# Optimization experiments

Hardware: AMD Instinct MI355X
Metric: run time of the kernel (lower is better)

Reference implementation:

```python
import jax, jax.numpy as jnp
import numpy as np

B, C, H, W = 4, 2048, 32, 32


def conv1x1(x, Wt, b):
    # 1x1 conv == per-pixel matmul over channels
    return jnp.einsum('oc,bchw->bohw', Wt, x) + b[None, :, None, None]


def cross_attention(Q, K, V):
    b, c, h, w = Q.shape
    q = Q.reshape(b, c, h * w)   # [B, C, N]
    k = K.reshape(b, c, h * w)
    v = V.reshape(b, c, h * w)
    scores = jnp.einsum('bcn,bcm->bnm', q, k) / jnp.sqrt(jnp.asarray(c, jnp.float32))
    attn = jax.nn.softmax(scores, axis=-1)          # [B, N, N]
    out = jnp.einsum('bcm,bnm->bcn', v, attn)       # V @ attn^T
    return out.reshape(b, c, h, w)


def setup_inputs() -> dict:
    key = jax.random.key(0)
    ks = jax.random.split(key, 14)
    d = {
        'F_rgb': jax.random.normal(ks[0], (B, C, H, W), jnp.float32),
        'F_indices': jax.random.normal(ks[1], (B, C, H, W), jnp.float32),
    }
    names = ['q_rgb', 'k_rgb', 'v_rgb', 'q_ind', 'k_ind', 'v_ind']
    for i, n in enumerate(names):
        d['W_' + n] = jax.random.normal(ks[2 + 2 * i], (C, C), jnp.float32) * 0.02
        d['b_' + n] = jax.random.normal(ks[3 + 2 * i], (C,), jnp.float32) * 0.01
    return d


def reference(F_rgb, F_indices, W_q_rgb, b_q_rgb, W_k_rgb, b_k_rgb, W_v_rgb, b_v_rgb,
              W_q_ind, b_q_ind, W_k_ind, b_k_ind, W_v_ind, b_v_ind):
    # RGB queries attend over index features
    Q_rgb = conv1x1(F_rgb, W_q_rgb, b_q_rgb)
    K_ind = conv1x1(F_indices, W_k_ind, b_k_ind)
    V_ind = conv1x1(F_indices, W_v_ind, b_v_ind)
    F_rgb_attended = cross_attention(Q_rgb, K_ind, V_ind)
    # Index queries attend over RGB features
    Q_ind = conv1x1(F_indices, W_q_ind, b_q_ind)
    K_rgb = conv1x1(F_rgb, W_k_rgb, b_k_rgb)
    V_rgb = conv1x1(F_rgb, W_v_rgb, b_v_rgb)
    F_ind_attended = cross_attention(Q_ind, K_rgb, V_rgb)
    F_final = F_rgb_attended + F_ind_attended
    attention_weights = jnp.stack([F_rgb_attended, F_ind_attended], axis=1)  # [B,2,C,H,W]
    # pre_attention_outputs is an identity passthrough of the inputs
    return (F_final, F_rgb, F_indices, attention_weights)
```

## Files before the change

### kernel.cpp

```cpp
#include <hip/hip_runtime.h>

typedef __bf16 bf16x8 __attribute__((ext_vector_type(8)));
typedef float  f32x4  __attribute__((ext_vector_type(4)));
typedef unsigned short u16;

__device__ __forceinline__ u16 f2bf(float f) {
  unsigned u = __builtin_bit_cast(unsigned, f);
  u += 0x7fffu + ((u >> 16) & 1u);
  return (u16)(u >> 16);
}
__device__ __forceinline__ float bf2f(u16 h) {
  return __builtin_bit_cast(float, (unsigned)h << 16);
}

using gvoid = __attribute__((address_space(1))) void;
using svoid = __attribute__((address_space(3))) void;
__device__ __forceinline__ void load_lds16(const void* g, void* s) {
  __builtin_amdgcn_global_load_lds((const gvoid*)g, (svoid*)s, 16, 0, 0);
}

__global__ void transpose_cvt(const float* __restrict__ Fr, const float* __restrict__ Fi,
                              u16* __restrict__ FTr, u16* __restrict__ FTi,
                              float* __restrict__ Or, float* __restrict__ Oi) {
  __shared__ float tile[32][33];
  const int b = blockIdx.z & 3;
  const bool ind = (blockIdx.z >= 4);
  const float* F = ind ? Fi : Fr;
  u16* FT = ind ? FTi : FTr;
  float* O = ind ? Oi : Or;
  const int n0 = blockIdx.x * 32, c0 = blockIdx.y * 32;
  const long boff = (long)b * 2048 * 1024;
  const float* Fb = F + boff;
  float* Ob = O + boff;
  u16* FTb = FT + (long)b * 1024 * 2048;
  const int tx = threadIdx.x, ty = threadIdx.y;
#pragma unroll
  for (int i = 0; i < 4; ++i) {
    const long idx = (long)(c0 + ty + i * 8) * 1024 + n0 + tx;
    float v = Fb[idx];
    tile[ty + i * 8][tx] = v;
    Ob[idx] = v;
  }
  __syncthreads();
#pragma unroll
  for (int i = 0; i < 4; ++i)
    FTb[(long)(n0 + ty + i * 8) * 2048 + c0 + tx] = f2bf(tile[tx][ty + i * 8]);
}

__global__ void cvt6(const float* __restrict__ s0, const float* __restrict__ s1,
                     const float* __restrict__ s2, const float* __restrict__ s3,
                     const float* __restrict__ s4, const float* __restrict__ s5,
                     u16* __restrict__ dst) {
  const int blk = blockIdx.x;
  const int chunk = blk >> 12;
  const int i = (blk & 4095) * 256 + threadIdx.x;
  const float* src;
  switch (chunk) {
    case 0: src = s0; break; case 1: src = s1; break; case 2: src = s2; break;
    case 3: src = s3; break; case 4: src = s4; break; default: src = s5; break;
  }
  float4 v = ((const float4*)src)[i];
  ushort4 o;
  o.x = f2bf(v.x); o.y = f2bf(v.y); o.z = f2bf(v.z); o.w = f2bf(v.w);
  ((ushort4*)(dst + (long)chunk * 4194304))[i] = o;
}


#define BAR_ do { asm volatile("" ::: "memory"); __builtin_amdgcn_s_barrier(); \
                  asm volatile("" ::: "memory"); } while (0)
#define SB0 __builtin_amdgcn_sched_barrier(0)
#define LGK0 asm volatile("s_waitcnt lgkmcnt(0)" ::: "memory")
#define VMW6 asm volatile("s_waitcnt vmcnt(6)" ::: "memory")

#define b0A0 0
#define b0A1 16384
#define b0B0 32768
#define b0B1 49152
#define b1A0 65536
#define b1A1 81920
#define b1B0 98304
#define b1B1 114688

#define STG(Mp, ld, row0, kt, off)                                                 \
  do {                                                                             \
    load_lds16(Mp + (long)((row0) + w * 8 + srow) * (ld) + (kt) * 64 + scol,       \
               sm + (off) + w * 1024);                                             \
    load_lds16(Mp + (long)((row0) + 64 + w * 8 + srow) * (ld) + (kt) * 64 + scol,  \
               sm + (off) + 8192 + w * 1024);                                      \
  } while (0)

#define RDA(off)                                                                   \
  _Pragma("unroll") for (int fm = 0; fm < 4; ++fm)                                 \
  _Pragma("unroll") for (int ks = 0; ks < 2; ++ks)                                 \
    fa[fm][ks] = *(const bf16x8*)(sm + (off) + aoff[fm] + kin[ks]);

#define RDB(off, dst)                                                              \
  _Pragma("unroll") for (int fn = 0; fn < 2; ++fn)                                 \
  _Pragma("unroll") for (int ks = 0; ks < 2; ++ks)                                 \
    dst[fn][ks] = *(const bf16x8*)(sm + (off) + boff[fn] + kin[ks]);

#define MMQ2(qa)                                                                   \
  __builtin_amdgcn_s_setprio(1);                                                   \
  _Pragma("unroll") for (int ks = 0; ks < 2; ++ks)                                 \
  _Pragma("unroll") for (int fm = 0; fm < 4; ++fm) {                               \
    _Pragma("unroll") for (int fn = 0; fn < 2; ++fn)                               \
      acc[qa][0][fm][fn] = __builtin_amdgcn_mfma_f32_16x16x32_bf16(                \
          fa[fm][ks], fb0[fn][ks], acc[qa][0][fm][fn], 0, 0, 0);                   \
    _Pragma("unroll") for (int fn = 0; fn < 2; ++fn)                               \
      acc[qa][1][fm][fn] = __builtin_amdgcn_mfma_f32_16x16x32_bf16(                \
          fa[fm][ks], fb1[fn][ks], acc[qa][1][fm][fn], 0, 0, 0);                   \
  }                                                                                \
  __builtin_amdgcn_s_setprio(0);

template <int OUT_BF16, int BIAS_MODE, int KSPLIT>
__global__ __launch_bounds__(512, 2) void gemm256(
    const u16* __restrict__ A0p, const u16* __restrict__ B0p, void* __restrict__ D0p,
    const float* __restrict__ ba0, const float* __restrict__ bb0,
    const u16* __restrict__ A1p, const u16* __restrict__ B1p, void* __restrict__ D1p,
    const float* __restrict__ ba1, const float* __restrict__ bb1,
    long sKH, int zsplit, int K, int lda, int ldb, int ldd,
    long sA, long sB, long sD) {
  __shared__ __attribute__((aligned(128))) char sm[131072];
  const int gx = gridDim.x, gy = gridDim.y;
  const int nwg = gx * gy * (int)gridDim.z;
  const int lin = blockIdx.x + gx * (blockIdx.y + gy * blockIdx.z);
  const int qch = nwg >> 3;
  int swzid = (lin & 7) * qch + (lin >> 3);
  const int bx = swzid % gx; swzid /= gx;
  const int by = swzid % gy;
  int zb = swzid / gy;
  int kh = 0;
  if (KSPLIT) { kh = zb >> 3; zb &= 7; }
  const bool s1 = (zb >= zsplit);
  const int zz = s1 ? zb - zsplit : zb;
  const u16* Ag = (s1 ? A1p : A0p) + (long)zz * sA + (long)kh * K;
  const u16* Bg = (s1 ? B1p : B0p) + (long)zz * sB + (long)kh * K;
  char* Dg = (char*)(s1 ? D1p : D0p) + (long)zz * sD * (OUT_BF16 ? 2 : 4)
           + (KSPLIT ? (long)kh * sKH : 0L);
  const float* ba = s1 ? ba1 : ba0;
  const float* bb = s1 ? bb1 : bb0;
  const int m0 = by * 256, n0 = bx * 256;
  const int t = threadIdx.x, w = t >> 6, l = t & 63;
  const int wr = w >> 2, wc = w & 3;
  const int lm = l & 15, lk = l >> 4;
  const int swz = (l & 7) << 4;
  const int srow = l >> 3;
  const int scol = ((l & 7) ^ srow) << 3;
  int aoff[4], boff[2], kin[2];
#pragma unroll
  for (int fm = 0; fm < 4; ++fm) aoff[fm] = (wr * 64 + fm * 16 + lm) * 128;
#pragma unroll
  for (int fn = 0; fn < 2; ++fn) boff[fn] = (wc * 32 + fn * 16 + lm) * 128;
  kin[0] = (lk * 16) ^ swz;
  kin[1] = (64 + lk * 16) ^ swz;

  f32x4 acc[2][2][4][2] = {};
  bf16x8 fa[4][2], fb0[2][2], fb1[2][2];

  const int nt = K >> 6;

  STG(Ag, lda, m0,       0, b0A0);
  STG(Bg, ldb, n0,       0, b0B0);
  STG(Bg, ldb, n0 + 128, 0, b0B1);
  STG(Ag, lda, m0 + 128, 0, b0A1);
  STG(Ag, lda, m0,       1, b1A0);
  STG(Bg, ldb, n0,       1, b1B0);
  STG(Bg, ldb, n0 + 128, 1, b1B1);
  VMW6;
  BAR_;

  for (int v = 0; v < nt; v += 2) {
    const int t2 = (v + 2 < nt) ? v + 2 : nt - 1;
    const int t3 = (v + 3 < nt) ? v + 3 : nt - 1;
    STG(Ag, lda, m0 + 128, v + 1, b1A1);
    RDA(b0A0); RDB(b0B0, fb0); RDB(b0B1, fb1);
    BAR_; LGK0; SB0; MMQ2(0);
    STG(Ag, lda, m0, t2, b0A0);
    STG(Bg, ldb, n0, t2, b0B0);
    STG(Bg, ldb, n0 + 128, t2, b0B1);
    RDA(b0A1);
    VMW6;
    BAR_; LGK0; SB0; MMQ2(1);
    STG(Ag, lda, m0 + 128, t2, b0A1);
    RDA(b1A0); RDB(b1B0, fb0); RDB(b1B1, fb1);
    BAR_; LGK0; SB0; MMQ2(0);
    STG(Ag, lda, m0, t3, b1A0);
    STG(Bg, ldb, n0, t3, b1B0);
    STG(Bg, ldb, n0 + 128, t3, b1B1);
    RDA(b1A1);
    VMW6;
    BAR_; LGK0; SB0; MMQ2(1);
  }

#pragma unroll
  for (int qa = 0; qa < 2; ++qa)
#pragma unroll
    for (int qb = 0; qb < 2; ++qb)
#pragma unroll
      for (int fm = 0; fm < 4; ++fm)
#pragma unroll
        for (int fn = 0; fn < 2; ++fn) {
          const int row0 = m0 + qa * 128 + wr * 64 + fm * 16 + lk * 4;
          const int col  = n0 + qb * 128 + wc * 32 + fn * 16 + lm;
          float cb = 0.f;
          if (BIAS_MODE == 1) cb = (col < 2048) ? ba[col] : bb[col - 2048];
          f32x4 vv = acc[qa][qb][fm][fn];
#pragma unroll
          for (int j = 0; j < 4; ++j) {
            float x = vv[j] + cb;
            if (BIAS_MODE == 2) x += ba[row0 + j];
            const long idx = (long)(row0 + j) * ldd + col;
            if (OUT_BF16) ((u16*)Dg)[idx] = f2bf(x);
            else          ((float*)Dg)[idx] = x;
          }
        }
}

__global__ void softmax_rows2(const u16* __restrict__ S0, const u16* __restrict__ S1,
                              u16* __restrict__ P, float alpha) {
  const long row = blockIdx.x;
  const int t = threadIdx.x, l = t & 63, w = t >> 6;
  ushort4 a = ((const ushort4*)(S0 + row * 1024))[t];
  ushort4 b = ((const ushort4*)(S1 + row * 1024))[t];
  float v0 = bf2f(a.x) + bf2f(b.x);
  float v1 = bf2f(a.y) + bf2f(b.y);
  float v2 = bf2f(a.z) + bf2f(b.z);
  float v3 = bf2f(a.w) + bf2f(b.w);
  __shared__ float red[8];
  float m = fmaxf(fmaxf(v0, v1), fmaxf(v2, v3));
#pragma unroll
  for (int off = 32; off; off >>= 1) m = fmaxf(m, __shfl_xor(m, off));
  if (l == 0) red[w] = m;
  __syncthreads();
  m = fmaxf(fmaxf(red[0], red[1]), fmaxf(red[2], red[3]));
  float e0 = __expf((v0 - m) * alpha);
  float e1 = __expf((v1 - m) * alpha);
  float e2 = __expf((v2 - m) * alpha);
  float e3 = __expf((v3 - m) * alpha);
  float s = e0 + e1 + e2 + e3;
#pragma unroll
  for (int off = 32; off; off >>= 1) s += __shfl_xor(s, off);
  if (l == 0) red[4 + w] = s;
  __syncthreads();
  s = red[4] + red[5] + red[6] + red[7];
  const float inv = 1.0f / s;
  ushort4 o;
  o.x = f2bf(e0 * inv); o.y = f2bf(e1 * inv);
  o.z = f2bf(e2 * inv); o.w = f2bf(e3 * inv);
  ((ushort4*)(P + row * 1024))[t] = o;
}

__global__ void final_add(const float4* __restrict__ aw, float4* __restrict__ dst) {
  const long i = (long)blockIdx.x * 256 + threadIdx.x;
  const long b = i >> 19;
  const long r = i & 524287;
  float4 a = aw[b * 1048576 + r];
  float4 c = aw[b * 1048576 + 524288 + r];
  float4 o;
  o.x = a.x + c.x; o.y = a.y + c.y; o.z = a.z + c.z; o.w = a.w + c.w;
  dst[i] = o;
}

extern "C" void kernel_launch(void* const* d_in, const int* in_sizes, int n_in,
                              void* d_out, int out_size, void* d_ws, size_t ws_size,
                              hipStream_t stream) {
  (void)in_sizes; (void)n_in; (void)out_size; (void)ws_size;
  const float* F_rgb = (const float*)d_in[0];
  const float* F_ind = (const float*)d_in[1];
  const float* bq_rgb = (const float*)d_in[3];
  const float* bk_rgb = (const float*)d_in[5];
  const float* bv_rgb = (const float*)d_in[7];
  const float* bq_ind = (const float*)d_in[9];
  const float* bk_ind = (const float*)d_in[11];
  const float* bv_ind = (const float*)d_in[13];

  char* ws = (char*)d_ws;
  u16* FT_rgb  = (u16*)(ws);
  u16* FT_ind  = (u16*)(ws + 16777216);
  u16* S1c     = (u16*)(ws);
  u16* Wall    = (u16*)(ws + 33554432);
  u16* Wqk_rgb = Wall;
  u16* Wqk_ind = (u16*)(ws + 50331648);
  u16* Wv_rgb  = (u16*)(ws + 67108864);
  u16* Wv_ind  = (u16*)(ws + 75497472);
  u16* QKT_rgb = (u16*)(ws + 83886080);
  u16* QKT_ind = (u16*)(ws + 117440512);
  u16* V_rgb   = (u16*)(ws + 150994944);
  u16* V_ind   = (u16*)(ws + 167772160);
  u16* S0c     = (u16*)(ws + 184549376);
  u16* P       = (u16*)(ws + 218103808);

  float* out       = (float*)d_out;
  float* out_final = out;
  float* out_Frgb  = out + 8388608;
  float* out_Find  = out + 16777216;
  float* AW        = out + 25165824;

  transpose_cvt<<<dim3(32, 64, 8), dim3(32, 8), 0, stream>>>(
      F_rgb, F_ind, FT_rgb, FT_ind, out_Frgb, out_Find);
  cvt6<<<24576, 256, 0, stream>>>((const float*)d_in[2], (const float*)d_in[4],
                                  (const float*)d_in[8], (const float*)d_in[10],
                                  (const float*)d_in[6], (const float*)d_in[12], Wall);

  gemm256<1, 1, 0><<<dim3(16, 4, 8), 512, 0, stream>>>(
      FT_rgb, Wqk_rgb, QKT_rgb, bq_rgb, bk_rgb,
      FT_ind, Wqk_ind, QKT_ind, bq_ind, bk_ind,
      0L, 4, 2048, 2048, 2048, 4096, 2097152L, 0L, 4194304L);

  gemm256<1, 2, 0><<<dim3(4, 8, 8), 512, 0, stream>>>(
      Wv_rgb, FT_rgb, V_rgb, bv_rgb, bv_rgb,
      Wv_ind, FT_ind, V_ind, bv_ind, bv_ind,
      0L, 4, 2048, 2048, 2048, 1024, 0L, 2097152L, 2097152L);

  gemm256<1, 0, 1><<<dim3(4, 4, 16), 512, 0, stream>>>(
      QKT_rgb, QKT_ind + 2048, S0c, nullptr, nullptr,
      QKT_ind, QKT_rgb + 2048, S0c + 4194304, nullptr, nullptr,
      (long)((char*)S1c - (char*)S0c), 4, 1024, 4096, 4096, 1024,
      4194304L, 4194304L, 1048576L);

  softmax_rows2<<<8192, 256, 0, stream>>>(S0c, S1c, P, 0.02209708691207961f);

  gemm256<0, 0, 0><<<dim3(4, 8, 8), 512, 0, stream>>>(
      V_ind, P, AW, nullptr, nullptr,
      V_rgb, P + 4194304, AW + 2097152, nullptr, nullptr,
      0L, 4, 1024, 1024, 1024, 1024, 2097152L, 1048576L, 4194304L);

  final_add<<<8192, 256, 0, stream>>>((const float4*)AW, (float4*)out_final);
}
```

Baseline: 329.4 us.

## Merge prep kernels and use smaller 128-tile GEMM for attention matmuls

Fuses the input transpose/convert kernel and the weight conversion kernel into one launch using extra grid z-slices. Adds a simpler 128x128-tile, 256-thread GEMM without multi-buffering and uses it for the scores GEMM and the attention-times-V GEMM. This gives those smaller GEMMs more blocks to fill the GPU's compute units, but gives up the deeper pipelining of the 256-tile kernel because each k-step waits on its loads before computing.

New measurement: 364.4 us. 10.6% more time.

```diff
diff --git a/kernel.cpp b/kernel.cpp
--- a/kernel.cpp
+++ b/kernel.cpp
@@ -19,9 +19,29 @@
   __builtin_amdgcn_global_load_lds((const gvoid*)g, (svoid*)s, 16, 0, 0);
 }
 
-__global__ void transpose_cvt(const float* __restrict__ Fr, const float* __restrict__ Fi,
-                              u16* __restrict__ FTr, u16* __restrict__ FTi,
-                              float* __restrict__ Or, float* __restrict__ Oi) {
+__global__ void prep(const float* __restrict__ Fr, const float* __restrict__ Fi,
+                     u16* __restrict__ FTr, u16* __restrict__ FTi,
+                     float* __restrict__ Or, float* __restrict__ Oi,
+                     const float* __restrict__ s0, const float* __restrict__ s1,
+                     const float* __restrict__ s2, const float* __restrict__ s3,
+                     const float* __restrict__ s4, const float* __restrict__ s5,
+                     u16* __restrict__ Wall) {
+  const int tx = threadIdx.x, ty = threadIdx.y;
+  if (blockIdx.z >= 8) {
+    const int gi = (blockIdx.z - 8) * 2048 + blockIdx.y * 32 + blockIdx.x;
+    const int chunk = gi >> 12;
+    const int i = (gi & 4095) * 256 + ty * 32 + tx;
+    const float* src;
+    switch (chunk) {
+      case 0: src = s0; break; case 1: src = s1; break; case 2: src = s2; break;
+      case 3: src = s3; break; case 4: src = s4; break; default: src = s5; break;
+    }
+    float4 v = ((const float4*)src)[i];
+    ushort4 o;
+    o.x = f2bf(v.x); o.y = f2bf(v.y); o.z = f2bf(v.z); o.w = f2bf(v.w);
+    ((ushort4*)(Wall + (long)chunk * 4194304))[i] = o;
+    return;
+  }
   __shared__ float tile[32][33];
   const int b = blockIdx.z & 3;
   const bool ind = (blockIdx.z >= 4);
@@ -33,7 +53,6 @@
   const float* Fb = F + boff;
   float* Ob = O + boff;
   u16* FTb = FT + (long)b * 1024 * 2048;
-  const int tx = threadIdx.x, ty = threadIdx.y;
 #pragma unroll
   for (int i = 0; i < 4; ++i) {
     const long idx = (long)(c0 + ty + i * 8) * 1024 + n0 + tx;
@@ -45,24 +64,6 @@
 #pragma unroll
   for (int i = 0; i < 4; ++i)
     FTb[(long)(n0 + ty + i * 8) * 2048 + c0 + tx] = f2bf(tile[tx][ty + i * 8]);
-}
-
-__global__ void cvt6(const float* __restrict__ s0, const float* __restrict__ s1,
-                     const float* __restrict__ s2, const float* __restrict__ s3,
-                     const float* __restrict__ s4, const float* __restrict__ s5,
-                     u16* __restrict__ dst) {
-  const int blk = blockIdx.x;
-  const int chunk = blk >> 12;
-  const int i = (blk & 4095) * 256 + threadIdx.x;
-  const float* src;
-  switch (chunk) {
-    case 0: src = s0; break; case 1: src = s1; break; case 2: src = s2; break;
-    case 3: src = s3; break; case 4: src = s4; break; default: src = s5; break;
-  }
-  float4 v = ((const float4*)src)[i];
-  ushort4 o;
-  o.x = f2bf(v.x); o.y = f2bf(v.y); o.z = f2bf(v.z); o.w = f2bf(v.w);
-  ((ushort4*)(dst + (long)chunk * 4194304))[i] = o;
 }
 
 
@@ -216,6 +217,90 @@
         }
 }
 
+template <int OUT_BF16, int KSPLIT>
+__global__ __launch_bounds__(256) void gemm128(
+    const u16* __restrict__ A0p, const u16* __restrict__ B0p, void* __restrict__ D0p,
+    const u16* __restrict__ A1p, const u16* __restrict__ B1p, void* __restrict__ D1p,
+    long sKH, int zsplit, int K, int lda, int ldb, int ldd,
+    long sA, long sB, long sD) {
+  __shared__ __attribute__((aligned(128))) char sm[32768];
+  char* sA_ = sm;
+  char* sB_ = sm + 16384;
+  int zb = blockIdx.z;
+  int kh = 0;
+  if (KSPLIT) { kh = zb >> 3; zb &= 7; }
+  const bool s1 = (zb >= zsplit);
+  const int zz = s1 ? zb - zsplit : zb;
+  const u16* Ab = (s1 ? A1p : A0p) + (long)zz * sA + (long)kh * K;
+  const u16* Bb = (s1 ? B1p : B0p) + (long)zz * sB + (long)kh * K;
+  char* Dg = (char*)(s1 ? D1p : D0p) + (long)zz * sD * (OUT_BF16 ? 2 : 4)
+           + (KSPLIT ? (long)kh * sKH : 0L);
+  const int m0 = blockIdx.y * 128, n0 = blockIdx.x * 128;
+  const int t = threadIdx.x;
+  const int w = t >> 6, l = t & 63;
+  const int wm = w >> 1, wn = w & 1;
+  const int lhi = l >> 4, llo = l & 15;
+  const int srow = l >> 3;
+  const int scolb = (((l & 7) ^ srow) << 4);
+  const int swz = (l & 7) << 4;
+  f32x4 acc[4][4] = {};
+  int abase[4], bbase[4];
+#pragma unroll
+  for (int f = 0; f < 4; ++f) {
+    abase[f] = (wm * 64 + f * 16 + llo) * 128;
+    bbase[f] = (wn * 64 + f * 16 + llo) * 128;
+  }
+  const int in0 = (0 * 64 + lhi * 16) ^ swz;
+  const int in1 = (1 * 64 + lhi * 16) ^ swz;
+
+  for (int k0 = 0; k0 < K; k0 += 64) {
+#pragma unroll
+    for (int i = 0; i < 4; ++i) {
+      const int ci = i * 4 + w;
+      const int row = ci * 8 + srow;
+      load_lds16((const char*)(Ab + (long)(m0 + row) * lda + k0) + scolb,
+                 sA_ + ci * 1024);
+      load_lds16((const char*)(Bb + (long)(n0 + row) * ldb + k0) + scolb,
+                 sB_ + ci * 1024);
+    }
+    asm volatile("s_waitcnt vmcnt(0)" ::: "memory");
+    __syncthreads();
+#pragma unroll
+    for (int ks = 0; ks < 2; ++ks) {
+      const int inner = ks ? in1 : in0;
+      bf16x8 af[4], bfr[4];
+#pragma unroll
+      for (int f = 0; f < 4; ++f) {
+        af[f]  = *(const bf16x8*)(sA_ + abase[f] + inner);
+        bfr[f] = *(const bf16x8*)(sB_ + bbase[f] + inner);
+      }
+#pragma unroll
+      for (int fm = 0; fm < 4; ++fm)
+#pragma unroll
+        for (int fn = 0; fn < 4; ++fn)
+          acc[fm][fn] = __builtin_amdgcn_mfma_f32_16x16x32_bf16(
+              af[fm], bfr[fn], acc[fm][fn], 0, 0, 0);
+    }
+    __syncthreads();
+  }
+
+#pragma unroll
+  for (int fm = 0; fm < 4; ++fm) {
+    const int row = m0 + wm * 64 + fm * 16 + lhi * 4;
+#pragma unroll
+    for (int fn = 0; fn < 4; ++fn) {
+      const int col = n0 + wn * 64 + fn * 16 + llo;
+      f32x4 v = acc[fm][fn];
+#pragma unroll
+      for (int j = 0; j < 4; ++j) {
+        const long idx = (long)(row + j) * ldd + col;
+        if (OUT_BF16) ((u16*)Dg)[idx] = f2bf(v[j]);
+        else          ((float*)Dg)[idx] = v[j];
+      }
+    }
+  }
+}
+
 __global__ void softmax_rows2(const u16* __restrict__ S0, const u16* __restrict__ S1,
                               u16* __restrict__ P, float alpha) {
   const long row = blockIdx.x;
@@ -296,11 +381,11 @@
   float* out_Find  = out + 16777216;
   float* AW        = out + 25165824;
 
-  transpose_cvt<<<dim3(32, 64, 8), dim3(32, 8), 0, stream>>>(
-      F_rgb, F_ind, FT_rgb, FT_ind, out_Frgb, out_Find);
-  cvt6<<<24576, 256, 0, stream>>>((const float*)d_in[2], (const float*)d_in[4],
-                                  (const float*)d_in[8], (const float*)d_in[10],
-                                  (const float*)d_in[6], (const float*)d_in[12], Wall);
+  prep<<<dim3(32, 64, 20), dim3(32, 8), 0, stream>>>(
+      F_rgb, F_ind, FT_rgb, FT_ind, out_Frgb, out_Find,
+      (const float*)d_in[2], (const float*)d_in[4],
+      (const float*)d_in[8], (const float*)d_in[10],
+      (const float*)d_in[6], (const float*)d_in[12], Wall);
 
   gemm256<1, 1, 0><<<dim3(16, 4, 8), 512, 0, stream>>>(
       FT_rgb, Wqk_rgb, QKT_rgb, bq_rgb, bk_rgb,
@@ -312,17 +397,17 @@
       Wv_ind, FT_ind, V_ind, bv_ind, bv_ind,
       0L, 4, 2048, 2048, 2048, 1024, 0L, 2097152L, 2097152L);
 
-  gemm256<1, 0, 1><<<dim3(4, 4, 16), 512, 0, stream>>>(
-      QKT_rgb, QKT_ind + 2048, S0c, nullptr, nullptr,
-      QKT_ind, QKT_rgb + 2048, S0c + 4194304, nullptr, nullptr,
+  gemm128<1, 1><<<dim3(8, 8, 16), 256, 0, stream>>>(
+      QKT_rgb, QKT_ind + 2048, S0c,
+      QKT_ind, QKT_rgb + 2048, S0c + 4194304,
       (long)((char*)S1c - (char*)S0c), 4, 1024, 4096, 4096, 1024,
       4194304L, 4194304L, 1048576L);
 
   softmax_rows2<<<8192, 256, 0, stream>>>(S0c, S1c, P, 0.02209708691207961f);
 
-  gemm256<0, 0, 0><<<dim3(4, 8, 8), 512, 0, stream>>>(
-      V_ind, P, AW, nullptr, nullptr,
-      V_rgb, P + 4194304, AW + 2097152, nullptr, nullptr,
+  gemm128<0, 0><<<dim3(8, 16, 8), 256, 0, stream>>>(
+      V_ind, P, AW,
+      V_rgb, P + 4194304, AW + 2097152,
       0L, 4, 1024, 1024, 1024, 1024, 2097152L, 1048576L, 4194304L);
 
   final_add<<<8192, 256, 0, stream>>>((const float4*)AW, (float4*)out_final);
```

## Split-K the score and PV GEMMs further and fuse the conversion kernels

Applied to the files above, without the earlier changes.

The transpose and weight-conversion kernels are merged into one launch. The QK^T score GEMM now splits K four ways instead of two, and softmax sums four bf16 partials. The PV GEMM is also split-K two ways with bf16 partial outputs, and a new final kernel reduces them into both the attention-weights and final outputs. The aim is more workgroups on the small GEMMs for better CU occupancy and one fewer launch. In exchange it adds bf16 rounding of partials, extra partial-buffer traffic and more complex workspace aliasing.

Result: slower. 358.9 us (+8.9%).

```diff
diff --git a/kernel.cpp b/kernel.cpp
--- a/kernel.cpp
+++ b/kernel.cpp
@@ -19,9 +19,29 @@
   __builtin_amdgcn_global_load_lds((const gvoid*)g, (svoid*)s, 16, 0, 0);
 }
 
-__global__ void transpose_cvt(const float* __restrict__ Fr, const float* __restrict__ Fi,
-                              u16* __restrict__ FTr, u16* __restrict__ FTi,
-                              float* __restrict__ Or, float* __restrict__ Oi) {
+__global__ void prep(const float* __restrict__ Fr, const float* __restrict__ Fi,
+                     u16* __restrict__ FTr, u16* __restrict__ FTi,
+                     float* __restrict__ Or, float* __restrict__ Oi,
+                     const float* __restrict__ s0, const float* __restrict__ s1,
+                     const float* __restrict__ s2, const float* __restrict__ s3,
+                     const float* __restrict__ s4, const float* __restrict__ s5,
+                     u16* __restrict__ Wall) {
+  const int tx = threadIdx.x, ty = threadIdx.y;
+  if (blockIdx.z >= 8) {
+    const int gi = (blockIdx.z - 8) * 2048 + blockIdx.y * 32 + blockIdx.x;
+    const int chunk = gi >> 12;
+    const int i = (gi & 4095) * 256 + ty * 32 + tx;
+    const float* src;
+    switch (chunk) {
+      case 0: src = s0; break; case 1: src = s1; break; case 2: src = s2; break;
+      case 3: src = s3; break; case 4: src = s4; break; default: src = s5; break;
+    }
+    float4 v = ((const float4*)src)[i];
+    ushort4 o;
+    o.x = f2bf(v.x); o.y = f2bf(v.y); o.z = f2bf(v.z); o.w = f2bf(v.w);
+    ((ushort4*)(Wall + (long)chunk * 4194304))[i] = o;
+    return;
+  }
   __shared__ float tile[32][33];
   const int b = blockIdx.z & 3;
   const bool ind = (blockIdx.z >= 4);
@@ -33,7 +53,6 @@
   const float* Fb = F + boff;
   float* Ob = O + boff;
   u16* FTb = FT + (long)b * 1024 * 2048;
-  const int tx = threadIdx.x, ty = threadIdx.y;
 #pragma unroll
   for (int i = 0; i < 4; ++i) {
     const long idx = (long)(c0 + ty + i * 8) * 1024 + n0 + tx;
@@ -45,24 +64,6 @@
 #pragma unroll
   for (int i = 0; i < 4; ++i)
     FTb[(long)(n0 + ty + i * 8) * 2048 + c0 + tx] = f2bf(tile[tx][ty + i * 8]);
-}
-
-__global__ void cvt6(const float* __restrict__ s0, const float* __restrict__ s1,
-                     const float* __restrict__ s2, const float* __restrict__ s3,
-                     const float* __restrict__ s4, const float* __restrict__ s5,
-                     u16* __restrict__ dst) {
-  const int blk = blockIdx.x;
-  const int chunk = blk >> 12;
-  const int i = (blk & 4095) * 256 + threadIdx.x;
-  const float* src;
-  switch (chunk) {
-    case 0: src = s0; break; case 1: src = s1; break; case 2: src = s2; break;
-    case 3: src = s3; break; case 4: src = s4; break; default: src = s5; break;
-  }
-  float4 v = ((const float4*)src)[i];
-  ushort4 o;
-  o.x = f2bf(v.x); o.y = f2bf(v.y); o.z = f2bf(v.z); o.w = f2bf(v.w);
-  ((ushort4*)(dst + (long)chunk * 4194304))[i] = o;
 }
 
 
@@ -118,7 +119,8 @@
     const float* __restrict__ ba0, const float* __restrict__ bb0,
     const u16* __restrict__ A1p, const u16* __restrict__ B1p, void* __restrict__ D1p,
     const float* __restrict__ ba1, const float* __restrict__ bb1,
-    long sKH, int zsplit, int K, int lda, int ldb, int ldd,
+    long sk1, long sk2, long sk3,
+    int zsplit, int K, int lda, int ldb, int ldd,
     long sA, long sB, long sD) {
   __shared__ __attribute__((aligned(128))) char sm[131072];
   const int gx = gridDim.x, gy = gridDim.y;
@@ -135,8 +137,10 @@
   const int zz = s1 ? zb - zsplit : zb;
   const u16* Ag = (s1 ? A1p : A0p) + (long)zz * sA + (long)kh * K;
   const u16* Bg = (s1 ? B1p : B0p) + (long)zz * sB + (long)kh * K;
-  char* Dg = (char*)(s1 ? D1p : D0p) + (long)zz * sD * (OUT_BF16 ? 2 : 4)
-           + (KSPLIT ? (long)kh * sKH : 0L);
+  long khoff = 0;
+  if (KSPLIT) { if (kh == 1) khoff = sk1; else if (kh == 2) khoff = sk2;
+                else if (kh == 3) khoff = sk3; }
+  char* Dg = (char*)(s1 ? D1p : D0p) + (long)zz * sD * (OUT_BF16 ? 2 : 4) + khoff;
   const float* ba = s1 ? ba1 : ba0;
   const float* bb = s1 ? bb1 : bb0;
   const int m0 = by * 256, n0 = bx * 256;
@@ -216,16 +220,19 @@
         }
 }
 
-__global__ void softmax_rows2(const u16* __restrict__ S0, const u16* __restrict__ S1,
+__global__ void softmax_rows4(const u16* __restrict__ S0, const u16* __restrict__ S1,
+                              const u16* __restrict__ S2, const u16* __restrict__ S3,
                               u16* __restrict__ P, float alpha) {
   const long row = blockIdx.x;
   const int t = threadIdx.x, l = t & 63, w = t >> 6;
   ushort4 a = ((const ushort4*)(S0 + row * 1024))[t];
   ushort4 b = ((const ushort4*)(S1 + row * 1024))[t];
-  float v0 = bf2f(a.x) + bf2f(b.x);
-  float v1 = bf2f(a.y) + bf2f(b.y);
-  float v2 = bf2f(a.z) + bf2f(b.z);
-  float v3 = bf2f(a.w) + bf2f(b.w);
+  ushort4 c = ((const ushort4*)(S2 + row * 1024))[t];
+  ushort4 d = ((const ushort4*)(S3 + row * 1024))[t];
+  float v0 = bf2f(a.x) + bf2f(b.x) + bf2f(c.x) + bf2f(d.x);
+  float v1 = bf2f(a.y) + bf2f(b.y) + bf2f(c.y) + bf2f(d.y);
+  float v2 = bf2f(a.z) + bf2f(b.z) + bf2f(c.z) + bf2f(d.z);
+  float v3 = bf2f(a.w) + bf2f(b.w) + bf2f(c.w) + bf2f(d.w);
   __shared__ float red[8];
   float m = fmaxf(fmaxf(v0, v1), fmaxf(v2, v3));
 #pragma unroll
@@ -250,15 +257,22 @@
   ((ushort4*)(P + row * 1024))[t] = o;
 }
 
-__global__ void final_add(const float4* __restrict__ aw, float4* __restrict__ dst) {
-  const long i = (long)blockIdx.x * 256 + threadIdx.x;
-  const long b = i >> 19;
-  const long r = i & 524287;
-  float4 a = aw[b * 1048576 + r];
-  float4 c = aw[b * 1048576 + 524288 + r];
-  float4 o;
-  o.x = a.x + c.x; o.y = a.y + c.y; o.z = a.z + c.z; o.w = a.w + c.w;
-  dst[i] = o;
+__global__ void final_add2(const ushort4* __restrict__ p00, const ushort4* __restrict__ p01,
+                           const ushort4* __restrict__ p10, const ushort4* __restrict__ p11,
+                           float4* __restrict__ aw, float4* __restrict__ ff) {
+  const long g = (long)blockIdx.x * 256 + threadIdx.x;
+  const long b = g >> 19;
+  const long rem = g & 524287;
+  ushort4 x0 = p00[g], y0 = p01[g], x1 = p10[g], y1 = p11[g];
+  float4 a0, a1, f;
+  a0.x = bf2f(x0.x) + bf2f(y0.x); a0.y = bf2f(x0.y) + bf2f(y0.y);
+  a0.z = bf2f(x0.z) + bf2f(y0.z); a0.w = bf2f(x0.w) + bf2f(y0.w);
+  a1.x = bf2f(x1.x) + bf2f(y1.x); a1.y = bf2f(x1.y) + bf2f(y1.y);
+  a1.z = bf2f(x1.z) + bf2f(y1.z); a1.w = bf2f(x1.w) + bf2f(y1.w);
+  f.x = a0.x + a1.x; f.y = a0.y + a1.y; f.z = a0.z + a1.z; f.w = a0.w + a1.w;
+  aw[(b * 2 + 0) * 524288 + rem] = a0;
+  aw[(b * 2 + 1) * 524288 + rem] = a1;
+  ff[b * 524288 + rem] = f;
 }
 
 extern "C" void kernel_launch(void* const* d_in, const int* in_sizes, int n_in,
@@ -277,7 +291,6 @@
   char* ws = (char*)d_ws;
   u16* FT_rgb  = (u16*)(ws);
   u16* FT_ind  = (u16*)(ws + 16777216);
-  u16* S1c     = (u16*)(ws);
   u16* Wall    = (u16*)(ws + 33554432);
   u16* Wqk_rgb = Wall;
   u16* Wqk_ind = (u16*)(ws + 50331648);
@@ -287,8 +300,15 @@
   u16* QKT_ind = (u16*)(ws + 117440512);
   u16* V_rgb   = (u16*)(ws + 150994944);
   u16* V_ind   = (u16*)(ws + 167772160);
-  u16* S0c     = (u16*)(ws + 184549376);
-  u16* P       = (u16*)(ws + 218103808);
+  u16* P       = (u16*)(ws + 184549376);
+  u16* Skh0    = (u16*)(ws + 201326592);
+  u16* Skh1    = (u16*)(ws + 218103808);
+  u16* Skh2    = (u16*)(ws);
+  u16* Skh3    = (u16*)(ws + 16777216);
+  u16* PV00    = (u16*)(ws + 201326592);
+  u16* PV01    = (u16*)(ws + 218103808);
+  u16* PV10    = (u16*)(ws);
+  u16* PV11    = (u16*)(ws + 16777216);
 
   float* out       = (float*)d_out;
   float* out_final = out;
@@ -296,34 +316,39 @@
   float* out_Find  = out + 16777216;
   float* AW        = out + 25165824;
 
-  transpose_cvt<<<dim3(32, 64, 8), dim3(32, 8), 0, stream>>>(
-      F_rgb, F_ind, FT_rgb, FT_ind, out_Frgb, out_Find);
-  cvt6<<<24576, 256, 0, stream>>>((const float*)d_in[2], (const float*)d_in[4],
-                                  (const float*)d_in[8], (const float*)d_in[10],
-                                  (const float*)d_in[6], (const float*)d_in[12], Wall);
+  prep<<<dim3(32, 64, 20), dim3(32, 8), 0, stream>>>(
+      F_rgb, F_ind, FT_rgb, FT_ind, out_Frgb, out_Find,
+      (const float*)d_in[2], (const float*)d_in[4],
+      (const float*)d_in[8], (const float*)d_in[10],
+      (const float*)d_in[6], (const float*)d_in[12], Wall);
 
   gemm256<1, 1, 0><<<dim3(16, 4, 8), 512, 0, stream>>>(
       FT_rgb, Wqk_rgb, QKT_rgb, bq_rgb, bk_rgb,
       FT_ind, Wqk_ind, QKT_ind, bq_ind, bk_ind,
-      0L, 4, 2048, 2048, 2048, 4096, 2097152L, 0L, 4194304L);
+      0L, 0L, 0L, 4, 2048, 2048, 2048, 4096, 2097152L, 0L, 4194304L);
 
   gemm256<1, 2, 0><<<dim3(4, 8, 8), 512, 0, stream>>>(
       Wv_rgb, FT_rgb, V_rgb, bv_rgb, bv_rgb,
       Wv_ind, FT_ind, V_ind, bv_ind, bv_ind,
-      0L, 4, 2048, 2048, 2048, 1024, 0L, 2097152L, 2097152L);
-
-  gemm256<1, 0, 1><<<dim3(4, 4, 16), 512, 0, stream>>>(
-      QKT_rgb, QKT_ind + 2048, S0c, nullptr, nullptr,
-      QKT_ind, QKT_rgb + 2048, S0c + 4194304, nullptr, nullptr,
-      (long)((char*)S1c - (char*)S0c), 4, 1024, 4096, 4096, 1024,
-      4194304L, 4194304L, 1048576L);
-
-  softmax_rows2<<<8192, 256, 0, stream>>>(S0c, S1c, P, 0.02209708691207961f);
-
-  gemm256<0, 0, 0><<<dim3(4, 8, 8), 512, 0, stream>>>(
-      V_ind, P, AW, nullptr, nullptr,
-      V_rgb, P + 4194304, AW + 2097152, nullptr, nullptr,
-      0L, 4, 1024, 1024, 1024, 1024, 2097152L, 1048576L, 4194304L);
-
-  final_add<<<8192, 256, 0, stream>>>((const float4*)AW, (float4*)out_final);
-}
+      0L, 0L, 0L, 4, 2048, 2048, 2048, 1024, 0L, 2097152L, 2097152L);
+
+  gemm256<1, 0, 1><<<dim3(4, 4, 32), 512, 0, stream>>>(
+      QKT_rgb, QKT_ind + 2048, Skh0, nullptr, nullptr,
+      QKT_ind, QKT_rgb + 2048, Skh0 + 4194304, nullptr, nullptr,
+      16777216L, -201326592L, -184549376L,
+      4, 512, 4096, 4096, 1024, 4194304L, 4194304L, 1048576L);
+
+  softmax_rows4<<<8192, 256, 0, stream>>>(Skh0, Skh1, Skh2, Skh3, P,
+                                          0.02209708691207961f);
+
+  gemm256<1, 0, 1><<<dim3(4, 8, 16), 512, 0, stream>>>(
+      V_ind, P, PV00, nullptr, nullptr,
+      V_rgb, P + 4194304, PV10, nullptr, nullptr,
+      16777216L, 0L, 0L,
+      4, 512, 1024, 1024, 1024, 2097152L, 1048576L, 2097152L);
+
+  final_add2<<<8192, 256, 0, stream>>>(
+      (const ushort4*)PV00, (const ushort4*)PV01,
+      (const ushort4*)PV10, (const ushort4*)PV11,
+      (float4*)AW, (float4*)out_final);
+}
```

## Stage GEMM epilogue through LDS for coalesced stores; merge prep kernels

Applied to the files above, without the earlier changes.

The GEMM epilogue now writes accumulators, with bias added, into shared memory one 64-row slab at a time. It then stores each slab to global memory as 16-byte row-contiguous vectors, replacing the scattered per-element stores. The transpose and weight-convert kernels are merged into one launch, and the transpose tile grows to 64 channels so each thread writes 8 bf16 values as one vector. This cuts uncoalesced global writes and one kernel launch, at the cost of extra barriers and LDS round trips in the epilogue.

After: 325.4 us, median of 2. Within noise of the previous version (-1.2%).

```diff
diff --git a/kernel.cpp b/kernel.cpp
--- a/kernel.cpp
+++ b/kernel.cpp
@@ -3,6 +3,7 @@
 typedef __bf16 bf16x8 __attribute__((ext_vector_type(8)));
 typedef float  f32x4  __attribute__((ext_vector_type(4)));
 typedef unsigned short u16;
+typedef unsigned short u16x8 __attribute__((ext_vector_type(8)));
 
 __device__ __forceinline__ u16 f2bf(float f) {
   unsigned u = __builtin_bit_cast(unsigned, f);
@@ -19,50 +20,54 @@
   __builtin_amdgcn_global_load_lds((const gvoid*)g, (svoid*)s, 16, 0, 0);
 }
 
-__global__ void transpose_cvt(const float* __restrict__ Fr, const float* __restrict__ Fi,
-                              u16* __restrict__ FTr, u16* __restrict__ FTi,
-                              float* __restrict__ Or, float* __restrict__ Oi) {
-  __shared__ float tile[32][33];
+__global__ void prep(const float* __restrict__ Fr, const float* __restrict__ Fi,
+                     u16* __restrict__ FTr, u16* __restrict__ FTi,
+                     float* __restrict__ Or, float* __restrict__ Oi,
+                     const float* __restrict__ s0, const float* __restrict__ s1,
+                     const float* __restrict__ s2, const float* __restrict__ s3,
+                     const float* __restrict__ s4, const float* __restrict__ s5,
+                     u16* __restrict__ Wall) {
+  const int tx = threadIdx.x, ty = threadIdx.y;
+  const int t2 = ty * 32 + tx;
+  if (blockIdx.z >= 8) {
+    const int gi = (blockIdx.z - 8) * 1024 + blockIdx.y * 32 + blockIdx.x;
+    const int chunk = gi >> 12;
+    const int i = (gi & 4095) * 256 + t2;
+    const float* src;
+    switch (chunk) {
+      case 0: src = s0; break; case 1: src = s1; break; case 2: src = s2; break;
+      case 3: src = s3; break; case 4: src = s4; break; default: src = s5; break;
+    }
+    float4 v = ((const float4*)src)[i];
+    ushort4 o;
+    o.x = f2bf(v.x); o.y = f2bf(v.y); o.z = f2bf(v.z); o.w = f2bf(v.w);
+    ((ushort4*)(Wall + (long)chunk * 4194304))[i] = o;
+    return;
+  }
+  __shared__ float tile[64][33];
   const int b = blockIdx.z & 3;
   const bool ind = (blockIdx.z >= 4);
   const float* F = ind ? Fi : Fr;
   u16* FT = ind ? FTi : FTr;
   float* O = ind ? Oi : Or;
-  const int n0 = blockIdx.x * 32, c0 = blockIdx.y * 32;
+  const int n0 = blockIdx.x * 32, c0 = blockIdx.y * 64;
   const long boff = (long)b * 2048 * 1024;
   const float* Fb = F + boff;
   float* Ob = O + boff;
   u16* FTb = FT + (long)b * 1024 * 2048;
-  const int tx = threadIdx.x, ty = threadIdx.y;
-#pragma unroll
-  for (int i = 0; i < 4; ++i) {
+#pragma unroll
+  for (int i = 0; i < 8; ++i) {
     const long idx = (long)(c0 + ty + i * 8) * 1024 + n0 + tx;
     float v = Fb[idx];
     tile[ty + i * 8][tx] = v;
     Ob[idx] = v;
   }
   __syncthreads();
-#pragma unroll
-  for (int i = 0; i < 4; ++i)
-    FTb[(long)(n0 + ty + i * 8) * 2048 + c0 + tx] = f2bf(tile[tx][ty + i * 8]);
-}
-
-__global__ void cvt6(const float* __restrict__ s0, const float* __restrict__ s1,
-                     const float* __restrict__ s2, const float* __restrict__ s3,
-                     const float* __restrict__ s4, const float* __restrict__ s5,
-                     u16* __restrict__ dst) {
-  const int blk = blockIdx.x;
-  const int chunk = blk >> 12;
-  const int i = (blk & 4095) * 256 + threadIdx.x;
-  const float* src;
-  switch (chunk) {
-    case 0: src = s0; break; case 1: src = s1; break; case 2: src = s2; break;
-    case 3: src = s3; break; case 4: src = s4; break; default: src = s5; break;
-  }
-  float4 v = ((const float4*)src)[i];
-  ushort4 o;
-  o.x = f2bf(v.x); o.y = f2bf(v.y); o.z = f2bf(v.z); o.w = f2bf(v.w);
-  ((ushort4*)(dst + (long)chunk * 4194304))[i] = o;
+  const int q = t2 & 7, r = t2 >> 3;
+  u16x8 o8;
+#pragma unroll
+  for (int k = 0; k < 8; ++k) o8[k] = f2bf(tile[8 * q + k][r]);
+  *(u16x8*)(FTb + (long)(n0 + r) * 2048 + c0 + 8 * q) = o8;
 }
 
 
@@ -71,6 +76,7 @@
 #define SB0 __builtin_amdgcn_sched_barrier(0)
 #define LGK0 asm volatile("s_waitcnt lgkmcnt(0)" ::: "memory")
 #define VMW6 asm volatile("s_waitcnt vmcnt(6)" ::: "memory")
+#define VMW0 asm volatile("s_waitcnt vmcnt(0)" ::: "memory")
 
 #define b0A0 0
 #define b0A1 16384
@@ -192,28 +198,45 @@
     BAR_; LGK0; SB0; MMQ2(1);
   }
 
+  VMW0;
+  const int esz = OUT_BF16 ? 2 : 4;
 #pragma unroll
   for (int qa = 0; qa < 2; ++qa)
 #pragma unroll
-    for (int qb = 0; qb < 2; ++qb)
-#pragma unroll
-      for (int fm = 0; fm < 4; ++fm)
+    for (int fm = 0; fm < 4; ++fm) {
+      BAR_;
+#pragma unroll
+      for (int qb = 0; qb < 2; ++qb)
 #pragma unroll
         for (int fn = 0; fn < 2; ++fn) {
-          const int row0 = m0 + qa * 128 + wr * 64 + fm * 16 + lk * 4;
-          const int col  = n0 + qb * 128 + wc * 32 + fn * 16 + lm;
-          float cb = 0.f;
-          if (BIAS_MODE == 1) cb = (col < 2048) ? ba[col] : bb[col - 2048];
-          f32x4 vv = acc[qa][qb][fm][fn];
+          const int col = qb * 128 + wc * 32 + fn * 16 + lm;
+          const f32x4 vv = acc[qa][qb][fm][fn];
 #pragma unroll
           for (int j = 0; j < 4; ++j) {
-            float x = vv[j] + cb;
-            if (BIAS_MODE == 2) x += ba[row0 + j];
-            const long idx = (long)(row0 + j) * ldd + col;
-            if (OUT_BF16) ((u16*)Dg)[idx] = f2bf(x);
-            else          ((float*)Dg)[idx] = x;
+            const int r = wr * 16 + lk * 4 + j;
+            float x = vv[j];
+            if (BIAS_MODE == 1) {
+              const int gc = n0 + col;
+              x += (gc < 2048) ? ba[gc] : bb[gc - 2048];
+            }
+            if (BIAS_MODE == 2)
+              x += ba[m0 + qa * 128 + wr * 64 + fm * 16 + lk * 4 + j];
+            if (OUT_BF16) ((u16*)sm)[r * 256 + col] = f2bf(x);
+            else          ((float*)sm)[r * 256 + col] = x;
           }
         }
+      LGK0;
+      BAR_;
+#pragma unroll
+      for (int p = 0; p < (OUT_BF16 ? 2 : 4); ++p) {
+        const int off = p * 8192 + t * 16;
+        const int r = OUT_BF16 ? (off >> 9) : (off >> 10);
+        const int inrow = OUT_BF16 ? (off & 511) : (off & 1023);
+        const int grow = m0 + qa * 128 + (r >> 4) * 64 + fm * 16 + (r & 15);
+        const f32x4 d = *(const f32x4*)(sm + off);
+        *(f32x4*)(Dg + ((long)grow * ldd + n0) * esz + inrow) = d;
+      }
+    }
 }
 
 __global__ void softmax_rows2(const u16* __restrict__ S0, const u16* __restrict__ S1,
@@ -296,11 +319,11 @@
   float* out_Find  = out + 16777216;
   float* AW        = out + 25165824;
 
-  transpose_cvt<<<dim3(32, 64, 8), dim3(32, 8), 0, stream>>>(
-      F_rgb, F_ind, FT_rgb, FT_ind, out_Frgb, out_Find);
-  cvt6<<<24576, 256, 0, stream>>>((const float*)d_in[2], (const float*)d_in[4],
-                                  (const float*)d_in[8], (const float*)d_in[10],
-                                  (const float*)d_in[6], (const float*)d_in[12], Wall);
+  prep<<<dim3(32, 32, 32), dim3(32, 8), 0, stream>>>(
+      F_rgb, F_ind, FT_rgb, FT_ind, out_Frgb, out_Find,
+      (const float*)d_in[2], (const float*)d_in[4],
+      (const float*)d_in[8], (const float*)d_in[10],
+      (const float*)d_in[6], (const float*)d_in[12], Wall);
 
   gemm256<1, 1, 0><<<dim3(16, 4, 8), 512, 0, stream>>>(
       FT_rgb, Wqk_rgb, QKT_rgb, bq_rgb, bk_rgb,
```
